# Performance work log

Hardware: AMD Instinct MI355X
Metric: run time of the kernel (lower is better)

Reference implementation:

```python
import itertools
import jax, jax.numpy as jnp
from jax import lax
import numpy as np

BS = 16          # block_size
PAD = 2          # split_tree padding = n_conv - 1
NCONV = 3
G = 4            # 4x4x4 grid of active coarse blocks
PADDED = BS + 2 * PAD + 2 * NCONV   # 26, tsdf slice / upsample size
SUB = BS // 2 + 2 * PAD             # 12, prev-block / sub-block spatial size
CIN = 32; COUT = 32
EPS = 1e-5
THRESH = 0.0     # gate: softmax(pred)[:, -1] > 0 is always True -> all blocks routed


def _conv(x, w):
    # torch Conv3d(k=3, s=1, p=0, bias=False)
    return lax.conv_general_dilated(x, w, (1, 1, 1), 'VALID',
                                    dimension_numbers=('NCDHW', 'OIDHW', 'NCDHW'))


def _bn_relu(x, g, b):
    # eval-mode BatchNorm3d (running_mean=0, running_var=1) + ReLU
    s = g * (1.0 / jnp.sqrt(1.0 + EPS))
    return jax.nn.relu(x * s[None, :, None, None, None] + b[None, :, None, None, None])


def _pool2(x):
    return lax.reduce_window(x, -jnp.inf, lax.max, (1, 1, 2, 2, 2), (1, 1, 2, 2, 2), 'VALID')


def setup_inputs() -> dict:
    key = jax.random.key(0)
    ks = jax.random.split(key, 12)
    N = G ** 3
    D = (G - 1) * BS + PADDED  # 74
    f = lambda k, s, sc=0.05: jax.random.normal(k, s, jnp.float32) * sc
    return {
        'prev_blocks': jax.random.normal(ks[0], (N, CIN, SUB, SUB, SUB), jnp.float32),
        'tsdf': jax.random.normal(ks[1], (1, 1, D, D, D), jnp.float32),
        'w_up': f(ks[2], (CIN, CIN, 4, 4, 4)),
        'w_c0': f(ks[3], (COUT, CIN + 1, 3, 3, 3)),
        'g_c0': jnp.ones(COUT, jnp.float32), 'b_c0': jnp.zeros(COUT, jnp.float32),
        'w_c1': f(ks[4], (COUT, COUT, 3, 3, 3)),
        'g_c1': jnp.ones(COUT, jnp.float32), 'b_c1': jnp.zeros(COUT, jnp.float32),
        'w_c2': f(ks[5], (COUT, COUT, 3, 3, 3)),
        'g_c2': jnp.ones(COUT, jnp.float32), 'b_c2': jnp.zeros(COUT, jnp.float32),
        'w_p0': f(ks[6], (16, CIN, 3, 3, 3)),
        'g_p0': jnp.ones(16, jnp.float32), 'b_p0': jnp.zeros(16, jnp.float32),
        'w_p1': f(ks[7], (8, 16, 3, 3, 3)),
        'g_p1': jnp.ones(8, jnp.float32), 'b_p1': jnp.zeros(8, jnp.float32),
        'w_lin': f(ks[8], (3, 8), 0.1),
        'b_lin': jnp.zeros(3, jnp.float32),
    }


def reference(prev_blocks, tsdf, w_up, w_c0, g_c0, b_c0, w_c1, g_c1, b_c1,
              w_c2, g_c2, b_c2, w_p0, g_p0, b_p0, w_p1, g_p1, b_p1, w_lin, b_lin):
    N = prev_blocks.shape[0]
    # --- PredictionBlock per coarse block, batched over all 64 blocks ---
    h = _pool2(_bn_relu(_conv(prev_blocks, w_p0), g_p0, b_p0))  # [N,16,5,5,5]
    h = _pool2(_bn_relu(_conv(h, w_p1), g_p1, b_p1))            # [N,8,1,1,1]
    pred = h.reshape(N, -1) @ w_lin.T + b_lin                   # [N,3]
    # gate (with thresh=0.0 every block is selected; computed for fidelity)
    gate = jax.nn.softmax(pred, axis=-1)[:, -1] > THRESH
    del gate
    # --- upsample selected (= all) blocks: ConvTranspose3d(k=4, s=2, p=0) ---
    up = lax.conv_transpose(prev_blocks, w_up, (2, 2, 2), 'VALID',
                            dimension_numbers=('NCDHW', 'IODHW', 'NCDHW'),
                            transpose_kernel=True)              # [N,CIN,26,26,26]
    # --- slice tsdf pyramid at each block's (x,y,z)*BS origin ---
    starts = jnp.asarray(np.array(list(itertools.product(range(G), repeat=3))) * BS,
                         jnp.int32)                              # [N,3]
    vol = tsdf[0, 0]
    slc = jax.vmap(lambda s: lax.dynamic_slice(vol, (s[0], s[1], s[2]),
                                               (PADDED, PADDED, PADDED)))(starts)
    x = jnp.concatenate([up, slc[:, None]], axis=1)              # [N,CIN+1,26,26,26]
    x = _bn_relu(_conv(x, w_c0), g_c0, b_c0)
    x = _bn_relu(_conv(x, w_c1), g_c1, b_c1)
    x = _bn_relu(_conv(x, w_c2), g_c2, b_c2)                     # [N,COUT,20,20,20]
    # --- split_tree: 8 overlapping children of size SUB per block ---
    n = (x.shape[-1] - 2 * PAD) // 2  # 8
    subs = jnp.stack([x[..., a:a + SUB, b:b + SUB, c:c + SUB]
                      for a, b, c in itertools.product((0, n), repeat=3)], axis=1)
    subtree = subs.reshape(-1, COUT, SUB, SUB, SUB)              # [8N,COUT,12,12,12]
    return (subtree, pred)
```

## Files before the change

kernel.cpp:

```cpp
#include <hip/hip_runtime.h>
#include <math.h>

#define NBLK 64
#define SUBTREE_FLOATS (512ull*32ull*1728ull)

typedef __attribute__((ext_vector_type(8))) short bf16x8;
typedef __attribute__((ext_vector_type(4))) float f32x4;

__device__ __forceinline__ unsigned short f2b(float f) {
    unsigned u = __float_as_uint(f);
    u = u + 0x7FFFu + ((u >> 16) & 1u);
    return (unsigned short)(u >> 16);
}
__device__ __forceinline__ float b2f(unsigned short h) {
    return __uint_as_float(((unsigned)h) << 16);
}
__device__ __forceinline__ float relu_bn(float acc, float g, float b) {
    float s = g * rsqrtf(1.0f + 1e-5f);
    float v = acc * s + b;
    return v > 0.f ? v : 0.f;
}
__device__ __forceinline__ int xcd_lin() {
    int bid = blockIdx.x, nwg = gridDim.x;
    if ((nwg & 7) == 0) {
        int per = nwg >> 3;
        return (bid & 7) * per + (bid >> 3);
    }
    return bid;
}

__global__ __launch_bounds__(128, 2)
void pred_p0(const float* __restrict__ prev, const float* __restrict__ w,
             const float* __restrict__ g, const float* __restrict__ b,
             float* __restrict__ h0) {
    int blk = blockIdx.x;
    int n = blk >> 4, co = blk & 15;
    int t = threadIdx.x;
    __shared__ float wlds[864];
    for (int i = t; i < 864; i += 128) wlds[i] = w[co * 864 + i];
    __syncthreads();
    __shared__ float pz5[10 * 10 * 5];
    if (t < 100) {
        int oy = t / 10, ox = t % 10;
        float acc[10];
        #pragma unroll
        for (int i = 0; i < 10; i++) acc[i] = 0.f;
        const float* pb = prev + (size_t)n * 32 * 1728;
        for (int ci = 0; ci < 32; ci++) {
            float wr[27];
            #pragma unroll
            for (int j = 0; j < 27; j++) wr[j] = wlds[ci * 27 + j];
            const float* pc = pb + ci * 1728;
            #pragma unroll
            for (int ky = 0; ky < 3; ky++) {
                #pragma unroll
                for (int kx = 0; kx < 3; kx++) {
                    const float* col = pc + (oy + ky) * 12 + (ox + kx);
                    #pragma unroll
                    for (int j = 0; j < 12; j++) {
                        float u = col[j * 144];
                        #pragma unroll
                        for (int kz = 0; kz < 3; kz++) {
                            int zz = j - kz;
                            if (zz >= 0 && zz < 10)
                                acc[zz] += u * wr[kz * 9 + ky * 3 + kx];
                        }
                    }
                }
            }
        }
        float sc = g[co] * rsqrtf(1.0f + 1e-5f);
        float bi = b[co];
        #pragma unroll
        for (int p = 0; p < 5; p++) {
            float a0 = acc[2 * p]     * sc + bi; a0 = a0 > 0.f ? a0 : 0.f;
            float a1 = acc[2 * p + 1] * sc + bi; a1 = a1 > 0.f ? a1 : 0.f;
            pz5[(oy * 10 + ox) * 5 + p] = fmaxf(a0, a1);
        }
    }
    __syncthreads();
    if (t < 125) {
        int pz = t / 25, py = (t / 5) % 5, px = t % 5;
        float m = -INFINITY;
        #pragma unroll
        for (int dy = 0; dy < 2; dy++)
        #pragma unroll
        for (int dx = 0; dx < 2; dx++)
            m = fmaxf(m, pz5[((2 * py + dy) * 10 + 2 * px + dx) * 5 + pz]);
        h0[(n * 16 + co) * 125 + pz * 25 + py * 5 + px] = m;
    }
}

__global__ void pred_p1(const float* __restrict__ h0, const float* __restrict__ w,
                        const float* __restrict__ g, const float* __restrict__ b,
                        const float* __restrict__ wlin, const float* __restrict__ blin,
                        float* __restrict__ pred_out) {
    int n = blockIdx.x;
    __shared__ float conv[216];
    __shared__ float pooled[8];
    int t = threadIdx.x;
    if (t < 216) {
        int co = t / 27, r = t % 27;
        int oz = r / 9, oy = (r / 3) % 3, ox = r % 3;
        float acc = 0.f;
        for (int ci = 0; ci < 16; ci++) {
            const float* hc = h0 + (n * 16 + ci) * 125 + oz * 25 + oy * 5 + ox;
            const float* wc = w + (co * 16 + ci) * 27;
            #pragma unroll
            for (int kz = 0; kz < 3; kz++)
            #pragma unroll
            for (int ky = 0; ky < 3; ky++)
            #pragma unroll
            for (int kx = 0; kx < 3; kx++)
                acc += hc[kz * 25 + ky * 5 + kx] * wc[kz * 9 + ky * 3 + kx];
        }
        conv[t] = relu_bn(acc, g[co], b[co]);
    }
    __syncthreads();
    if (t < 8) {
        float m = -INFINITY;
        for (int dz = 0; dz < 2; dz++)
        for (int dy = 0; dy < 2; dy++)
        for (int dx = 0; dx < 2; dx++)
            m = fmaxf(m, conv[t * 27 + dz * 9 + dy * 3 + dx]);
        pooled[t] = m;
    }
    __syncthreads();
    if (t < 3) {
        float acc = blin[t];
        #pragma unroll
        for (int j = 0; j < 8; j++) acc += pooled[j] * wlin[t * 8 + j];
        pred_out[n * 3 + t] = acc;
    }
}

__global__ __launch_bounds__(256)
void ptcvt(const float* __restrict__ prev, unsigned short* __restrict__ Pt) {
    int n = blockIdx.x;
    const float* pb = prev + (size_t)n * 32 * 1728;
    unsigned short* ob = Pt + (size_t)n * 2744 * 32;
    for (int pos = threadIdx.x; pos < 2744; pos += 256) {
        int x = pos % 14, y = (pos / 14) % 14, zz = pos / 196;
        ushort4* o = (ushort4*)(ob + (size_t)pos * 32);
        if (x >= 1 && x <= 12 && y >= 1 && y <= 12 && zz >= 1 && zz <= 12) {
            int src = (zz - 1) * 144 + (y - 1) * 12 + (x - 1);
            unsigned short v[32];
            #pragma unroll
            for (int ci = 0; ci < 32; ci++) v[ci] = f2b(pb[(size_t)ci * 1728 + src]);
            #pragma unroll
            for (int j = 0; j < 8; j++)
                o[j] = make_ushort4(v[4 * j], v[4 * j + 1], v[4 * j + 2], v[4 * j + 3]);
        } else {
            #pragma unroll
            for (int j = 0; j < 8; j++) o[j] = make_ushort4(0, 0, 0, 0);
        }
    }
}

__global__ void wupprep(const float* __restrict__ wup, unsigned short* __restrict__ Wt) {
    int i = blockIdx.x * 256 + threadIdx.x;
    int tap = i >> 10, rem = i & 1023, co = rem >> 5, ci = rem & 31;
    Wt[i] = f2b(wup[co * 2048 + ci * 64 + tap]);
}

__global__ __launch_bounds__(256, 2)
void ups_mfma(const unsigned short* __restrict__ Pt,
              const unsigned short* __restrict__ Wt,
              unsigned short* __restrict__ Ut, int n0)
{
    constexpr int TPW = 11;
    int lin = xcd_lin();
    int z  = lin % 26;
    int nl = lin / 26;
    int lane = threadIdx.x & 63, wave = threadIdx.x >> 6;
    int ln = lane & 15, quad = lane >> 4;
    int pz = z & 1, izb = (z >> 1) + 1;
    int py = wave >> 1, px = wave & 1;

    const unsigned short* pbase =
        Pt + (size_t)(n0 + nl) * 2744 * 32 + (size_t)izb * 196 * 32 + quad * 8;

    int nidx[TPW];
    const unsigned short* bptr[TPW];
    #pragma unroll
    for (int t = 0; t < TPW; t++) {
        int n = t * 16 + ln;
        nidx[t] = (n < 169) ? n : 169;
        int nc = (n < 169) ? n : 168;
        int iy = nc / 13 + 1, ix = nc % 13 + 1;
        bptr[t] = pbase + ((size_t)iy * 14 + ix) * 32;
    }
    f32x4 acc[TPW][2];
    #pragma unroll
    for (int t = 0; t < TPW; t++) {
        acc[t][0] = (f32x4){0.f, 0.f, 0.f, 0.f};
        acc[t][1] = (f32x4){0.f, 0.f, 0.f, 0.f};
    }

    #pragma unroll 1
    for (int tap = 0; tap < 8; tap++) {
        int dz = tap >> 2, dy = (tap >> 1) & 1, dx = tap & 1;
        int ptap = (pz + 2 * dz) * 16 + (py + 2 * dy) * 4 + (px + 2 * dx);
        const unsigned short* wp = Wt + ptap * 1024 + ln * 32 + quad * 8;
        bf16x8 Af0 = *(const bf16x8*)wp;
        bf16x8 Af1 = *(const bf16x8*)(wp + 512);
        int off = -((dz * 196 + dy * 14 + dx) * 32);
        #pragma unroll
        for (int t = 0; t < TPW; t++) {
            bf16x8 Bf = *(const bf16x8*)(bptr[t] + off);
            acc[t][0] = __builtin_amdgcn_mfma_f32_16x16x32_bf16(Af0, Bf, acc[t][0], 0, 0, 0);
            acc[t][1] = __builtin_amdgcn_mfma_f32_16x16x32_bf16(Af1, Bf, acc[t][1], 0, 0, 0);
        }
    }

    #pragma unroll
    for (int t = 0; t < TPW; t++) {
        if (nidx[t] >= 169) continue;
        int oy = py + 2 * (nidx[t] / 13);
        int ox = px + 2 * (nidx[t] % 13);
        unsigned short* o = Ut +
            ((size_t)nl * 17576 + (size_t)z * 676 + oy * 26 + ox) * 32 + quad * 4;
        *(ushort4*)o = make_ushort4(f2b(acc[t][0][0]), f2b(acc[t][0][1]),
                                    f2b(acc[t][0][2]), f2b(acc[t][0][3]));
        *(ushort4*)(o + 16) = make_ushort4(f2b(acc[t][1][0]), f2b(acc[t][1][1]),
                                           f2b(acc[t][1][2]), f2b(acc[t][1][3]));
    }
}

__global__ void wprep(const float* __restrict__ w, unsigned short* __restrict__ Wt,
                      int wstride) {
    int i = blockIdx.x * 256 + threadIdx.x;
    if (i >= 27648) return;
    int tap = i >> 10, rem = i & 1023, co = rem >> 5, ci = rem & 31;
    Wt[i] = f2b(w[co * wstride + ci * 27 + tap]);
}

__global__ __launch_bounds__(128)
void vkern(const float* __restrict__ tsdf, const float* __restrict__ w_c0,
           unsigned short* __restrict__ V) {
    int yy = blockIdx.x % 72, zz = blockIdx.x / 72;
    int xx = threadIdx.x;
    if (xx >= 72) return;
    float tv[27];
    #pragma unroll
    for (int kz = 0; kz < 3; kz++)
    #pragma unroll
    for (int ky = 0; ky < 3; ky++)
    #pragma unroll
    for (int kx = 0; kx < 3; kx++)
        tv[kz * 9 + ky * 3 + kx] = tsdf[(size_t)(zz + kz) * 5476 + (yy + ky) * 74 + (xx + kx)];
    unsigned short* o = V + (((size_t)zz * 72 + yy) * 72 + xx) * 32;
    for (int co = 0; co < 32; co++) {
        float a = 0.f;
        const float* wc = w_c0 + co * 891 + 864;
        #pragma unroll
        for (int j = 0; j < 27; j++) a += tv[j] * wc[j];
        o[co] = f2b(a);
    }
}

template<int SIN, int SOUT, int MODE, int TPW>
__global__ __launch_bounds__(256, 2)
void conv_mfma(const unsigned short* __restrict__ in_t,
               const unsigned short* __restrict__ Wt,
               const float* __restrict__ gg, const float* __restrict__ bb,
               unsigned short* __restrict__ out_t, float* __restrict__ out_f,
               const unsigned short* __restrict__ V, int n0)
{
    constexpr int NPOS = SOUT * SOUT;
    constexpr int NT = (NPOS + 15) / 16;
    int lin = xcd_lin();
    int z  = lin % SOUT;
    int nl = lin / SOUT;
    int lane = threadIdx.x & 63, wave = threadIdx.x >> 6;
    int ln = lane & 15, quad = lane >> 4;

    int nidx[TPW], py[TPW], px[TPW];
    const unsigned short* bptr[TPW];
    const unsigned short* inb =
        in_t + (size_t)nl * SIN * SIN * SIN * 32 + (size_t)z * SIN * SIN * 32;
    #pragma unroll
    for (int t = 0; t < TPW; t++) {
        int ti = wave + 4 * t;
        int n = ti * 16 + ln;
        nidx[t] = (ti < NT && n < NPOS) ? n : NPOS;
        int nc = (nidx[t] < NPOS) ? nidx[t] : (NPOS - 1);
        py[t] = nc / SOUT; px[t] = nc % SOUT;
        bptr[t] = inb + ((size_t)py[t] * SIN + px[t]) * 32 + quad * 8;
    }
    f32x4 acc[TPW][2];
    if constexpr (MODE == 1) {
        int n = n0 + nl;
        int A = (n >> 4) * 16, B = ((n >> 2) & 3) * 16, C = (n & 3) * 16;
        #pragma unroll
        for (int t = 0; t < TPW; t++) {
            const unsigned short* vp =
                V + (((size_t)(A + z) * 72 + (B + py[t])) * 72 + (C + px[t])) * 32 + quad * 4;
            ushort4 v0 = *(const ushort4*)vp;
            ushort4 v1 = *(const ushort4*)(vp + 16);
            acc[t][0][0] = b2f(v0.x); acc[t][0][1] = b2f(v0.y);
            acc[t][0][2] = b2f(v0.z); acc[t][0][3] = b2f(v0.w);
            acc[t][1][0] = b2f(v1.x); acc[t][1][1] = b2f(v1.y);
            acc[t][1][2] = b2f(v1.z); acc[t][1][3] = b2f(v1.w);
        }
    } else {
        #pragma unroll
        for (int t = 0; t < TPW; t++) {
            #pragma unroll
            for (int c = 0; c < 2; c++)
                acc[t][c] = (f32x4){0.f, 0.f, 0.f, 0.f};
        }
    }

    const unsigned short* wp0 = Wt + ln * 32 + quad * 8;
    bf16x8 A0 = *(const bf16x8*)wp0;
    bf16x8 A1 = *(const bf16x8*)(wp0 + 512);
    bf16x8 B[TPW];
    #pragma unroll
    for (int t = 0; t < TPW; t++) B[t] = *(const bf16x8*)bptr[t];

    #pragma unroll 1
    for (int tap = 0; tap < 27; tap++) {
        int nt = tap < 26 ? tap + 1 : 26;
        int kz = nt / 9, ky = (nt % 9) / 3, kx = nt % 3;
        const unsigned short* wp = Wt + nt * 1024 + ln * 32 + quad * 8;
        bf16x8 An0 = *(const bf16x8*)wp;
        bf16x8 An1 = *(const bf16x8*)(wp + 512);
        size_t off = ((size_t)kz * SIN * SIN + (size_t)ky * SIN + kx) * 32;
        bf16x8 Bn[TPW];
        #pragma unroll
        for (int t = 0; t < TPW; t++) Bn[t] = *(const bf16x8*)(bptr[t] + off);
        #pragma unroll
        for (int t = 0; t < TPW; t++) {
            acc[t][0] = __builtin_amdgcn_mfma_f32_16x16x32_bf16(A0, B[t], acc[t][0], 0, 0, 0);
            acc[t][1] = __builtin_amdgcn_mfma_f32_16x16x32_bf16(A1, B[t], acc[t][1], 0, 0, 0);
        }
        A0 = An0; A1 = An1;
        #pragma unroll
        for (int t = 0; t < TPW; t++) B[t] = Bn[t];
    }

    int cobase = quad * 4;
    f32x4 g0 = *(const f32x4*)(gg + cobase);
    f32x4 g1 = *(const f32x4*)(gg + 16 + cobase);
    f32x4 b0 = *(const f32x4*)(bb + cobase);
    f32x4 b1 = *(const f32x4*)(bb + 16 + cobase);

    #pragma unroll
    for (int t = 0; t < TPW; t++) {
        if (nidx[t] >= NPOS) continue;
        float v0[4], v1[4];
        #pragma unroll
        for (int r = 0; r < 4; r++) {
            v0[r] = relu_bn(acc[t][0][r], g0[r], b0[r]);
            v1[r] = relu_bn(acc[t][1][r], g1[r], b1[r]);
        }
        if constexpr (MODE != 2) {
            unsigned short* o = out_t +
                ((size_t)nl * SOUT * SOUT * SOUT + (size_t)z * NPOS + nidx[t]) * 32 + cobase;
            *(ushort4*)o        = make_ushort4(f2b(v0[0]), f2b(v0[1]), f2b(v0[2]), f2b(v0[3]));
            *(ushort4*)(o + 16) = make_ushort4(f2b(v1[0]), f2b(v1[1]), f2b(v1[2]), f2b(v1[3]));
        } else {
            int n = n0 + nl;
            int oy = py[t], ox = px[t];
            #pragma unroll
            for (int za = 0; za < 2; za++) {
                int zz = z - za * 8; if (zz < 0 || zz >= 12) continue;
                #pragma unroll
                for (int yb = 0; yb < 2; yb++) {
                    int yy = oy - yb * 8; if (yy < 0 || yy >= 12) continue;
                    #pragma unroll
                    for (int xc = 0; xc < 2; xc++) {
                        int xx = ox - xc * 8; if (xx < 0 || xx >= 12) continue;
                        int s = za * 4 + yb * 2 + xc;
                        float* ob = out_f + ((size_t)n * 8 + s) * 32 * 1728
                                    + zz * 144 + yy * 12 + xx;
                        #pragma unroll
                        for (int r = 0; r < 4; r++) {
                            ob[(size_t)(cobase + r) * 1728]      = v0[r];
                            ob[(size_t)(16 + cobase + r) * 1728] = v1[r];
                        }
                    }
                }
            }
        }
    }
}

extern "C" void kernel_launch(void* const* d_in, const int* in_sizes, int n_in,
                              void* d_out, int out_size, void* d_ws, size_t ws_size,
                              hipStream_t stream) {
    const float* prev  = (const float*)d_in[0];
    const float* tsdf  = (const float*)d_in[1];
    const float* w_up  = (const float*)d_in[2];
    const float* w_c0  = (const float*)d_in[3];
    const float* g_c0  = (const float*)d_in[4];
    const float* b_c0  = (const float*)d_in[5];
    const float* w_c1  = (const float*)d_in[6];
    const float* g_c1  = (const float*)d_in[7];
    const float* b_c1  = (const float*)d_in[8];
    const float* w_c2  = (const float*)d_in[9];
    const float* g_c2  = (const float*)d_in[10];
    const float* b_c2  = (const float*)d_in[11];
    const float* w_p0  = (const float*)d_in[12];
    const float* g_p0  = (const float*)d_in[13];
    const float* b_p0  = (const float*)d_in[14];
    const float* w_p1  = (const float*)d_in[15];
    const float* g_p1  = (const float*)d_in[16];
    const float* b_p1  = (const float*)d_in[17];
    const float* w_lin = (const float*)d_in[18];
    const float* b_lin = (const float*)d_in[19];

    float* out = (float*)d_out;
    char* wsb  = (char*)d_ws;

    size_t off = 0;
    float* h0 = (float*)(wsb + off);            off += 512000;
    unsigned short* Wt0 = (unsigned short*)(wsb + off); off += 55296;
    unsigned short* Wt1 = (unsigned short*)(wsb + off); off += 55296;
    unsigned short* Wt2 = (unsigned short*)(wsb + off); off += 55296;
    unsigned short* V   = (unsigned short*)(wsb + off); off += 23887872;
    unsigned short* Pt  = (unsigned short*)(wsb + off); off += 11239424;
    unsigned short* WupT= (unsigned short*)(wsb + off); off += 131072;
    size_t fixed = off;

    int chunk = 64;
    while (chunk > 1) {
        size_t need = fixed + (size_t)chunk *
            (1124864ull  + 884736ull  + 681472ull );
        if (need <= ws_size) break;
        chunk >>= 1;
    }
    unsigned short* U_t = (unsigned short*)(wsb + off); off += (size_t)chunk * 1124864;
    unsigned short* X0t = (unsigned short*)(wsb + off); off += (size_t)chunk * 884736;
    unsigned short* X1t = (unsigned short*)(wsb + off);

    pred_p0<<<64 * 16, 128, 0, stream>>>(prev, w_p0, g_p0, b_p0, h0);
    pred_p1<<<64, 256, 0, stream>>>(h0, w_p1, g_p1, b_p1, w_lin, b_lin,
                                    out + SUBTREE_FLOATS);
    ptcvt<<<64, 256, 0, stream>>>(prev, Pt);
    wupprep<<<256, 256, 0, stream>>>(w_up, WupT);
    wprep<<<108, 256, 0, stream>>>(w_c0, Wt0, 891);
    wprep<<<108, 256, 0, stream>>>(w_c1, Wt1, 864);
    wprep<<<108, 256, 0, stream>>>(w_c2, Wt2, 864);
    vkern<<<72 * 72, 128, 0, stream>>>(tsdf, w_c0, V);

    for (int n0 = 0; n0 < NBLK; n0 += chunk) {
        ups_mfma<<<chunk * 26, 256, 0, stream>>>(Pt, WupT, U_t, n0);
        conv_mfma<26, 24, 1, 9><<<chunk * 24, 256, 0, stream>>>(
            U_t, Wt0, g_c0, b_c0, X0t, nullptr, V, n0);
        conv_mfma<24, 22, 0, 8><<<chunk * 22, 256, 0, stream>>>(
            X0t, Wt1, g_c1, b_c1, X1t, nullptr, nullptr, n0);
        conv_mfma<22, 20, 2, 7><<<chunk * 20, 256, 0, stream>>>(
            X1t, Wt2, g_c2, b_c2, nullptr, out, nullptr, n0);
    }
}
```

Before: 701.9 us.

## Tile conv over 4 output z-slices to reuse input rows across kz taps

Restructures the MFMA conv kernel so each workgroup computes a block of 4 consecutive output z-slices for 2 position tiles per wave, instead of one z-slice with many position tiles. Each loaded input z-row is fed to up to 3 kz weight taps, so B-operand loads drop from 27 per output slice to 6 per 4 slices. The grid is now indexed by position-tile group, z-block and batch, with tail handling for SOUT values not divisible by 4. In exchange it holds 16 accumulators plus 6 weight fragments per wave, raising register pressure, and drops the software prefetch of the next tap.

```diff
diff --git a/kernel.cpp b/kernel.cpp
--- a/kernel.cpp
+++ b/kernel.cpp
@@ -259,7 +259,7 @@
     }
 }
 
-template<int SIN, int SOUT, int MODE, int TPW>
+template<int SIN, int SOUT, int MODE, int TG>
 __global__ __launch_bounds__(256, 2)
 void conv_mfma(const unsigned short* __restrict__ in_t,
                const unsigned short* __restrict__ Wt,
@@ -269,75 +269,91 @@
 {
     constexpr int NPOS = SOUT * SOUT;
     constexpr int NT = (NPOS + 15) / 16;
+    constexpr int ZB = (SOUT + 3) / 4;
+    constexpr bool ZEXACT = (SOUT % 4) == 0;
     int lin = xcd_lin();
-    int z  = lin % SOUT;
-    int nl = lin / SOUT;
+    int tg = lin % TG;
+    int zb = (lin / TG) % ZB;
+    int nl = lin / (TG * ZB);
+    int z0 = zb * 4;
+    int zcnt = ZEXACT ? 4 : ((SOUT - z0) < 4 ? (SOUT - z0) : 4);
     int lane = threadIdx.x & 63, wave = threadIdx.x >> 6;
     int ln = lane & 15, quad = lane >> 4;
 
-    int nidx[TPW], py[TPW], px[TPW];
-    const unsigned short* bptr[TPW];
-    const unsigned short* inb =
-        in_t + (size_t)nl * SIN * SIN * SIN * 32 + (size_t)z * SIN * SIN * 32;
-    #pragma unroll
-    for (int t = 0; t < TPW; t++) {
-        int ti = wave + 4 * t;
+    int nidx[2], py[2], px[2];
+    const unsigned short* bptr[2];
+    const unsigned short* inb = in_t + (size_t)nl * SIN * SIN * SIN * 32;
+    #pragma unroll
+    for (int t = 0; t < 2; t++) {
+        int ti = tg * 8 + wave * 2 + t;
         int n = ti * 16 + ln;
         nidx[t] = (ti < NT && n < NPOS) ? n : NPOS;
         int nc = (nidx[t] < NPOS) ? nidx[t] : (NPOS - 1);
         py[t] = nc / SOUT; px[t] = nc % SOUT;
         bptr[t] = inb + ((size_t)py[t] * SIN + px[t]) * 32 + quad * 8;
     }
-    f32x4 acc[TPW][2];
+
+    f32x4 acc[4][2][2];
     if constexpr (MODE == 1) {
         int n = n0 + nl;
-        int A = (n >> 4) * 16, B = ((n >> 2) & 3) * 16, C = (n & 3) * 16;
-        #pragma unroll
-        for (int t = 0; t < TPW; t++) {
-            const unsigned short* vp =
-                V + (((size_t)(A + z) * 72 + (B + py[t])) * 72 + (C + px[t])) * 32 + quad * 4;
-            ushort4 v0 = *(const ushort4*)vp;
-            ushort4 v1 = *(const ushort4*)(vp + 16);
-            acc[t][0][0] = b2f(v0.x); acc[t][0][1] = b2f(v0.y);
-            acc[t][0][2] = b2f(v0.z); acc[t][0][3] = b2f(v0.w);
-            acc[t][1][0] = b2f(v1.x); acc[t][1][1] = b2f(v1.y);
-            acc[t][1][2] = b2f(v1.z); acc[t][1][3] = b2f(v1.w);
+        int Ab = (n >> 4) * 16, Bb = ((n >> 2) & 3) * 16, Cb = (n & 3) * 16;
+        #pragma unroll
+        for (int zc = 0; zc < 4; zc++) {
+            int zo = z0 + zc;
+            #pragma unroll
+            for (int t = 0; t < 2; t++) {
+                const unsigned short* vp =
+                    V + (((size_t)(Ab + zo) * 72 + (Bb + py[t])) * 72 + (Cb + px[t])) * 32
+                      + quad * 4;
+                ushort4 v0 = *(const ushort4*)vp;
+                ushort4 v1 = *(const ushort4*)(vp + 16);
+                acc[zc][t][0][0] = b2f(v0.x); acc[zc][t][0][1] = b2f(v0.y);
+                acc[zc][t][0][2] = b2f(v0.z); acc[zc][t][0][3] = b2f(v0.w);
+                acc[zc][t][1][0] = b2f(v1.x); acc[zc][t][1][1] = b2f(v1.y);
+                acc[zc][t][1][2] = b2f(v1.z); acc[zc][t][1][3] = b2f(v1.w);
+            }
         }
     } else {
         #pragma unroll
-        for (int t = 0; t < TPW; t++) {
-            #pragma unroll
-            for (int c = 0; c < 2; c++)
-                acc[t][c] = (f32x4){0.f, 0.f, 0.f, 0.f};
-        }
-    }
-
-    const unsigned short* wp0 = Wt + ln * 32 + quad * 8;
-    bf16x8 A0 = *(const bf16x8*)wp0;
-    bf16x8 A1 = *(const bf16x8*)(wp0 + 512);
-    bf16x8 B[TPW];
-    #pragma unroll
-    for (int t = 0; t < TPW; t++) B[t] = *(const bf16x8*)bptr[t];
+        for (int zc = 0; zc < 4; zc++)
+        #pragma unroll
+        for (int t = 0; t < 2; t++)
+        #pragma unroll
+        for (int c = 0; c < 2; c++)
+            acc[zc][t][c] = (f32x4){0.f, 0.f, 0.f, 0.f};
+    }
 
     #pragma unroll 1
-    for (int tap = 0; tap < 27; tap++) {
-        int nt = tap < 26 ? tap + 1 : 26;
-        int kz = nt / 9, ky = (nt % 9) / 3, kx = nt % 3;
-        const unsigned short* wp = Wt + nt * 1024 + ln * 32 + quad * 8;
-        bf16x8 An0 = *(const bf16x8*)wp;
-        bf16x8 An1 = *(const bf16x8*)(wp + 512);
-        size_t off = ((size_t)kz * SIN * SIN + (size_t)ky * SIN + kx) * 32;
-        bf16x8 Bn[TPW];
-        #pragma unroll
-        for (int t = 0; t < TPW; t++) Bn[t] = *(const bf16x8*)(bptr[t] + off);
-        #pragma unroll
-        for (int t = 0; t < TPW; t++) {
-            acc[t][0] = __builtin_amdgcn_mfma_f32_16x16x32_bf16(A0, B[t], acc[t][0], 0, 0, 0);
-            acc[t][1] = __builtin_amdgcn_mfma_f32_16x16x32_bf16(A1, B[t], acc[t][1], 0, 0, 0);
-        }
-        A0 = An0; A1 = An1;
-        #pragma unroll
-        for (int t = 0; t < TPW; t++) B[t] = Bn[t];
+    for (int kyx = 0; kyx < 9; kyx++) {
+        int ky = kyx / 3, kx = kyx % 3;
+        const unsigned short* wp = Wt + (size_t)kyx * 1024 + ln * 32 + quad * 8;
+        bf16x8 A[3][2];
+        #pragma unroll
+        for (int kz = 0; kz < 3; kz++) {
+            A[kz][0] = *(const bf16x8*)(wp + (size_t)kz * 9216);
+            A[kz][1] = *(const bf16x8*)(wp + (size_t)kz * 9216 + 512);
+        }
+        size_t xyo = ((size_t)ky * SIN + kx) * 32;
+        #pragma unroll
+        for (int j = 0; j < 6; j++) {
+            int zia = z0 + j;
+            int zs = zia < SIN ? zia : SIN - 1;
+            size_t off = (size_t)zs * SIN * SIN * 32 + xyo;
+            bf16x8 B0 = *(const bf16x8*)(bptr[0] + off);
+            bf16x8 B1 = *(const bf16x8*)(bptr[1] + off);
+            #pragma unroll
+            for (int kz = 0; kz < 3; kz++) {
+                constexpr int dummy = 0; (void)dummy;
+                int zc = j - kz;
+                if (zc < 0 || zc >= 4) continue;
+                if (ZEXACT || zc < zcnt) {
+                    acc[zc][0][0] = __builtin_amdgcn_mfma_f32_16x16x32_bf16(A[kz][0], B0, acc[zc][0][0], 0, 0, 0);
+                    acc[zc][0][1] = __builtin_amdgcn_mfma_f32_16x16x32_bf16(A[kz][1], B0, acc[zc][0][1], 0, 0, 0);
+                    acc[zc][1][0] = __builtin_amdgcn_mfma_f32_16x16x32_bf16(A[kz][0], B1, acc[zc][1][0], 0, 0, 0);
+                    acc[zc][1][1] = __builtin_amdgcn_mfma_f32_16x16x32_bf16(A[kz][1], B1, acc[zc][1][1], 0, 0, 0);
+                }
+            }
+        }
     }
 
     int cobase = quad * 4;
@@ -347,38 +363,43 @@
     f32x4 b1 = *(const f32x4*)(bb + 16 + cobase);
 
     #pragma unroll
-    for (int t = 0; t < TPW; t++) {
-        if (nidx[t] >= NPOS) continue;
-        float v0[4], v1[4];
-        #pragma unroll
-        for (int r = 0; r < 4; r++) {
-            v0[r] = relu_bn(acc[t][0][r], g0[r], b0[r]);
-            v1[r] = relu_bn(acc[t][1][r], g1[r], b1[r]);
-        }
-        if constexpr (MODE != 2) {
-            unsigned short* o = out_t +
-                ((size_t)nl * SOUT * SOUT * SOUT + (size_t)z * NPOS + nidx[t]) * 32 + cobase;
-            *(ushort4*)o        = make_ushort4(f2b(v0[0]), f2b(v0[1]), f2b(v0[2]), f2b(v0[3]));
-            *(ushort4*)(o + 16) = make_ushort4(f2b(v1[0]), f2b(v1[1]), f2b(v1[2]), f2b(v1[3]));
-        } else {
-            int n = n0 + nl;
-            int oy = py[t], ox = px[t];
-            #pragma unroll
-            for (int za = 0; za < 2; za++) {
-                int zz = z - za * 8; if (zz < 0 || zz >= 12) continue;
+    for (int zc = 0; zc < 4; zc++) {
+        if (!ZEXACT && zc >= zcnt) continue;
+        int zo = z0 + zc;
+        #pragma unroll
+        for (int t = 0; t < 2; t++) {
+            if (nidx[t] >= NPOS) continue;
+            float v0[4], v1[4];
+            #pragma unroll
+            for (int r = 0; r < 4; r++) {
+                v0[r] = relu_bn(acc[zc][t][0][r], g0[r], b0[r]);
+                v1[r] = relu_bn(acc[zc][t][1][r], g1[r], b1[r]);
+            }
+            if constexpr (MODE != 2) {
+                unsigned short* o = out_t +
+                    ((size_t)nl * SOUT * SOUT * SOUT + (size_t)zo * NPOS + nidx[t]) * 32 + cobase;
+                *(ushort4*)o        = make_ushort4(f2b(v0[0]), f2b(v0[1]), f2b(v0[2]), f2b(v0[3]));
+                *(ushort4*)(o + 16) = make_ushort4(f2b(v1[0]), f2b(v1[1]), f2b(v1[2]), f2b(v1[3]));
+            } else {
+                int n = n0 + nl;
+                int oy = py[t], ox = px[t];
                 #pragma unroll
-                for (int yb = 0; yb < 2; yb++) {
-                    int yy = oy - yb * 8; if (yy < 0 || yy >= 12) continue;
+                for (int za = 0; za < 2; za++) {
+                    int zz = zo - za * 8; if (zz < 0 || zz >= 12) continue;
                     #pragma unroll
-                    for (int xc = 0; xc < 2; xc++) {
-                        int xx = ox - xc * 8; if (xx < 0 || xx >= 12) continue;
-                        int s = za * 4 + yb * 2 + xc;
-                        float* ob = out_f + ((size_t)n * 8 + s) * 32 * 1728
-                                    + zz * 144 + yy * 12 + xx;
+                    for (int yb = 0; yb < 2; yb++) {
+                        int yy = oy - yb * 8; if (yy < 0 || yy >= 12) continue;
                         #pragma unroll
-                        for (int r = 0; r < 4; r++) {
-                            ob[(size_t)(cobase + r) * 1728]      = v0[r];
-                            ob[(size_t)(16 + cobase + r) * 1728] = v1[r];
+                        for (int xc = 0; xc < 2; xc++) {
+                            int xx = ox - xc * 8; if (xx < 0 || xx >= 12) continue;
+                            int s = za * 4 + yb * 2 + xc;
+                            float* ob = out_f + ((size_t)n * 8 + s) * 32 * 1728
+                                        + zz * 144 + yy * 12 + xx;
+                            #pragma unroll
+                            for (int r = 0; r < 4; r++) {
+                                ob[(size_t)(cobase + r) * 1728]      = v0[r];
+                                ob[(size_t)(16 + cobase + r) * 1728] = v1[r];
+                            }
                         }
                     }
                 }
@@ -447,11 +468,11 @@
 
     for (int n0 = 0; n0 < NBLK; n0 += chunk) {
         ups_mfma<<<chunk * 26, 256, 0, stream>>>(Pt, WupT, U_t, n0);
-        conv_mfma<26, 24, 1, 9><<<chunk * 24, 256, 0, stream>>>(
+        conv_mfma<26, 24, 1, 5><<<chunk * 30, 256, 0, stream>>>(
             U_t, Wt0, g_c0, b_c0, X0t, nullptr, V, n0);
-        conv_mfma<24, 22, 0, 8><<<chunk * 22, 256, 0, stream>>>(
+        conv_mfma<24, 22, 0, 4><<<chunk * 24, 256, 0, stream>>>(
             X0t, Wt1, g_c1, b_c1, X1t, nullptr, nullptr, n0);
-        conv_mfma<22, 20, 2, 7><<<chunk * 20, 256, 0, stream>>>(
+        conv_mfma<22, 20, 2, 4><<<chunk * 20, 256, 0, stream>>>(
             X1t, Wt2, g_c2, b_c2, nullptr, out, nullptr, n0);
     }
 }
```

New measurement: 650.0 us. -7.4%, faster.
